# Optimization experiments

Measured on AMD Instinct MI355X. Metric: run time of the kernel, lower is better.

Reference implementation:

```python
import jax, jax.numpy as jnp
import numpy as np

BS, S, D, N, E = 16, 8, 10, 32, 300
H, STATE_DIM, MID, OC = 128, 96, 256, 100

def setup_inputs():
    ks = jax.random.split(jax.random.key(0), 24)
    g = lambda i, shape: (0.02 * jax.random.normal(ks[i], shape)).astype(jnp.float32)
    return {
        "stock_news": jax.random.normal(ks[0], (BS, S, D, N, E), dtype=jnp.float32),
        "stock_feats": jax.random.normal(ks[1], (BS, STATE_DIM), dtype=jnp.float32),
        "conv_w3": g(2, (S, OC, E, 3)), "conv_b3": g(3, (S, OC)),
        "conv_w4": g(4, (S, OC, E, 4)), "conv_b4": g(5, (S, OC)),
        "conv_w5": g(6, (S, OC, E, 5)), "conv_b5": g(7, (S, OC)),
        "w_ih": g(8, (S, 4 * H, 3 * OC)), "w_hh": g(9, (S, 4 * H, H)),
        "b_ih": g(10, (S, 4 * H)), "b_hh": g(11, (S, 4 * H)),
        "linX_w": g(12, (S, H, 2 * H)), "linX_b": g(13, (S, H)),
        "linY_w": g(14, (S, 64, H)), "linY_b": g(15, (S, 64)),
        "w1": g(16, (24, STATE_DIM)), "b1": g(17, (24,)),
        "w2": g(18, (16, 24)), "b2": g(19, (16,)),
        "arch_w1": g(20, (MID, 16 + 64 * S)), "arch_b1": g(21, (MID,)),
        "arch_w2": g(22, (S, MID)), "arch_b2": g(23, (S,)),
        "action_var": jnp.full((S,), -0.25, dtype=jnp.float32),
    }

def _conv_maxpool(x, w, b, k):
    # x: [S,B,D,N,E], w: [S,OC,E,k] -> conv1d over news axis then max-pool -> [S,B,D,OC]
    L = x.shape[3] - k + 1
    y = jnp.broadcast_to(b[:, None, None, None, :], (x.shape[0], x.shape[1], x.shape[2], L, w.shape[1]))
    for j in range(k):
        y = y + jnp.einsum('sbdne,soe->sbdno', x[:, :, :, j:j + L, :], w[:, :, :, j])
    return y.max(axis=3)

def _lstm_attn(xs, w_ih, w_hh, b_ih, b_hh):
    # single-stock LSTM (batch_first) + attention from original code; xs: [B,D,I] -> [B,2H]
    pre = jnp.einsum('bdi,gi->dbg', xs, w_ih) + b_ih + b_hh  # [D,B,4H]
    h0 = jnp.zeros((xs.shape[0], w_hh.shape[1]), xs.dtype)
    def step(carry, g_t):
        h, c = carry
        gates = g_t + h @ w_hh.T
        i, f, g, o = jnp.split(gates, 4, axis=-1)  # PyTorch gate order i,f,g,o
        c = jax.nn.sigmoid(f) * c + jax.nn.sigmoid(i) * jnp.tanh(g)
        h = jax.nn.sigmoid(o) * jnp.tanh(c)
        return (h, c), h
    (hn, _), outs = jax.lax.scan(step, (h0, h0), pre)
    outs = outs.transpose(1, 0, 2)  # [B,D,H]
    w = jnp.einsum('bh,bdh->bd', hn, outs)[:, None, :]  # [B,1,D]
    w = jax.nn.softmax(w, axis=1)  # softmax over singleton dim, exactly as torch code (yields ones)
    out = jnp.sum(w.transpose(0, 2, 1) * outs, axis=1)  # [B,H]
    return jnp.concatenate([hn, out], axis=-1)  # [B,2H]

def _forward(stock_news, stock_feats, conv_w3, conv_b3, conv_w4, conv_b4, conv_w5, conv_b5,
             w_ih, w_hh, b_ih, b_hh, linX_w, linX_b, linY_w, linY_b,
             w1, b1, w2, b2, arch_w1, arch_b1, arch_w2, arch_b2, action_var):
    x = stock_news.transpose(1, 0, 2, 3, 4)  # [S,B,D,N,E]
    feats = [_conv_maxpool(x, w, b, k) for (w, b, k) in
             ((conv_w3, conv_b3, 3), (conv_w4, conv_b4, 4), (conv_w5, conv_b5, 5))]
    text = jnp.concatenate(feats, axis=-1)  # [S,B,D,300]
    comb = jax.vmap(_lstm_attn)(text, w_ih, w_hh, b_ih, b_hh)  # [S,B,2H]
    hX = jax.nn.relu(jnp.einsum('sbi,shi->sbh', comb, linX_w) + linX_b[:, None, :])  # dropout is eval-mode identity
    hY = jax.nn.relu(jnp.einsum('sbh,soh->sbo', hX, linY_w) + linY_b[:, None, :])  # [S,B,64]
    stock_text = hY.transpose(1, 0, 2).reshape(stock_news.shape[0], -1)  # [B,S*64]
    f = jax.nn.relu(stock_feats @ w1.T + b1) @ w2.T + b2  # [B,16]
    total = jnp.concatenate([stock_text, f], axis=-1)  # [B,16+64S]
    mu = jnp.tanh(jax.nn.relu(total @ arch_w1.T + arch_b1) @ arch_w2.T + arch_b2)
    return mu, jnp.exp(action_var)

def reference(stock_news, stock_feats, conv_w3, conv_b3, conv_w4, conv_b4, conv_w5, conv_b5,
              w_ih, w_hh, b_ih, b_hh, linX_w, linX_b, linY_w, linY_b,
              w1, b1, w2, b2, arch_w1, arch_b1, arch_w2, arch_b2, action_var):
    return _forward(stock_news, stock_feats, conv_w3, conv_b3, conv_w4, conv_b4, conv_w5, conv_b5,
                    w_ih, w_hh, b_ih, b_hh, linX_w, linX_b, linY_w, linY_b,
                    w1, b1, w2, b2, arch_w1, arch_b1, arch_w2, arch_b2, action_var)
```

## Files before the change

kernel.cpp:

```cpp
#include <hip/hip_runtime.h>
#include <math.h>

#define S_   8
#define B_   16
#define D_   10
#define N_   32
#define E_   300
#define H_   128
#define G4_  512
#define SDIM_ 96
#define MID_ 256
#define TOT_ 528

#define NWPACK 3850240
#define NWPRE  1310720

typedef unsigned short u16;
typedef __attribute__((ext_vector_type(8))) short short8;
typedef __attribute__((ext_vector_type(4))) short short4v;
typedef __attribute__((ext_vector_type(4))) float f32x4;

static __device__ __forceinline__ u16 f2bf(float f) {
    unsigned u = __builtin_bit_cast(unsigned, f);
    return (u16)((u + 0x7FFFu + ((u >> 16) & 1u)) >> 16);
}

__global__ void prep(const float* __restrict__ w3, const float* __restrict__ b3,
                     const float* __restrict__ w4, const float* __restrict__ b4,
                     const float* __restrict__ w5, const float* __restrict__ b5,
                     const float* __restrict__ w_ih,
                     u16* __restrict__ wpack2, u16* __restrict__ wpre2,
                     float* __restrict__ bcomb) {
    int idx = blockIdx.x * blockDim.x + threadIdx.x;
    if (idx < NWPACK) {
        int j = idx & 7, q = (idx >> 3) & 3;
        int rest = idx >> 5;
        int c = rest % 320, ks = (rest / 320) % 47, s = rest / 15040;
        int kk = ks * 32 + q * 8 + j;
        int tap = kk / 300, e = kk - tap * 300;
        float v = 0.f;
        if (tap < 5) {
            if (c < 100)      { if (tap < 3) v = w3[((s*100 + c      )*300 + e)*3 + tap]; }
            else if (c < 200) { if (tap < 4) v = w4[((s*100 + c - 100)*300 + e)*4 + tap]; }
            else if (c < 300) {              v = w5[((s*100 + c - 200)*300 + e)*5 + tap]; }
        }
        wpack2[idx] = f2bf(v);
    } else if (idx < NWPACK + NWPRE) {
        int i2 = idx - NWPACK;
        int j = i2 & 7, q = (i2 >> 3) & 3;
        int rest = i2 >> 5;
        int g = rest & 511, ks = (rest >> 9) % 10, s = rest / 5120;
        int kk = ks * 32 + q * 8 + j;
        float v = (kk < 300) ? w_ih[((size_t)s * 512 + g) * 300 + kk] : 0.f;
        wpre2[i2] = f2bf(v);
    }
    if (idx < 2560) {
        int c = idx % 320, s = idx / 320;
        float bv = 0.f;
        if (c < 100)      bv = b3[s*100 + c];
        else if (c < 200) bv = b4[s*100 + c - 100];
        else if (c < 300) bv = b5[s*100 + c - 200];
        bcomb[idx] = bv;
    }
}

__global__ __launch_bounds__(256, 3) void conv_mfma(const float* __restrict__ news,
                                                    const u16* __restrict__ wpack2,
                                                    const float* __restrict__ bcomb,
                                                    u16* __restrict__ text_bf) {
    __shared__ u16 xs[2 * 10816];
    const int tid = threadIdx.x, bid = blockIdx.x;
    const int s = bid & 7, b2d = bid >> 3, b2 = b2d / 10, d = b2d % 10;
    const int l = tid & 63, w = tid >> 6, q = l >> 4, r16 = l & 15;

    const u16* gp[5];
#pragma unroll
    for (int nt = 0; nt < 5; ++nt) {
        int c = w * 80 + nt * 16 + r16;
        gp[nt] = wpack2 + (size_t)s * 481280 + c * 32 + q * 8;
    }

    short8 bf0[5], bf1[5];
#pragma unroll
    for (int nt = 0; nt < 5; ++nt) bf0[nt] = *reinterpret_cast<const short8*>(gp[nt]);
#pragma unroll
    for (int nt = 0; nt < 5; ++nt) bf1[nt] = *reinterpret_cast<const short8*>(gp[nt] + 10240);

#pragma unroll
    for (int sm = 0; sm < 2; ++sm) {
        const float4* xg = reinterpret_cast<const float4*>(
            news + (size_t)(((b2 * 2 + sm) * 8 + s) * 10 + d) * 9600);
        for (int i = tid; i < 2704; i += 256) {
            ushort4 u;
            if (i < 2400) {
                float4 v = xg[i];
                u.x = f2bf(v.x); u.y = f2bf(v.y); u.z = f2bf(v.z); u.w = f2bf(v.w);
            } else { u.x = 0; u.y = 0; u.z = 0; u.w = 0; }
            *reinterpret_cast<ushort4*>(&xs[sm * 10816 + 4 * i]) = u;
        }
    }
    __syncthreads();

    f32x4 acc[4][5];
#pragma unroll
    for (int m = 0; m < 4; ++m)
#pragma unroll
        for (int nt = 0; nt < 5; ++nt) acc[m][nt] = (f32x4)(0.f);

#define LOADA(dst, ks) do {                                                     \
    _Pragma("unroll")                                                           \
    for (int m_ = 0; m_ < 4; ++m_) {                                            \
        int off_ = (m_ >> 1) * 10816 + ((m_ & 1) * 16 + r16) * 300 + (ks) * 32 + q * 8; \
        short4v lo_ = *reinterpret_cast<const short4v*>(&xs[off_]);             \
        short4v hi_ = *reinterpret_cast<const short4v*>(&xs[off_ + 4]);         \
        dst[m_] = __builtin_shufflevector(lo_, hi_, 0, 1, 2, 3, 4, 5, 6, 7);    \
    } } while (0)

#define MFMAS(bfv, av) do {                                                     \
    __builtin_amdgcn_s_setprio(1);                                              \
    _Pragma("unroll")                                                           \
    for (int m_ = 0; m_ < 4; ++m_)                                              \
        _Pragma("unroll")                                                       \
        for (int nt_ = 0; nt_ < 5; ++nt_)                                       \
            acc[m_][nt_] = __builtin_amdgcn_mfma_f32_16x16x32_bf16(av[m_], bfv[nt_], acc[m_][nt_], 0, 0, 0); \
    __builtin_amdgcn_s_setprio(0);                                              \
    } while (0)

    for (int ks = 0; ks < 46; ks += 2) {
        short8 a0[4], a1[4];
        LOADA(a0, ks);
        MFMAS(bf0, a0);
#pragma unroll
        for (int nt = 0; nt < 5; ++nt)
            bf0[nt] = *reinterpret_cast<const short8*>(gp[nt] + (ks + 2) * 10240);

        LOADA(a1, ks + 1);
        MFMAS(bf1, a1);
        if (ks + 3 < 47) {
#pragma unroll
            for (int nt = 0; nt < 5; ++nt)
                bf1[nt] = *reinterpret_cast<const short8*>(gp[nt] + (ks + 3) * 10240);
        }
    }
    {
        short8 a0[4];
        LOADA(a0, 46);
        MFMAS(bf0, a0);
    }
#undef LOADA
#undef MFMAS

#pragma unroll
    for (int sm = 0; sm < 2; ++sm) {
        const size_t trow = ((size_t)(s * 16 + b2 * 2 + sm) * 10 + d) * 320;
#pragma unroll
        for (int nt = 0; nt < 5; ++nt) {
            int oc = w * 80 + nt * 16 + r16;
            int L = (oc < 100) ? 30 : (oc < 200) ? 29 : 28;
            float mx = -3e38f;
#pragma unroll
            for (int r = 0; r < 4; ++r) {
                mx = fmaxf(mx, acc[sm * 2][nt][r]);
                int row1 = 16 + q * 4 + r;
                if (row1 < L) mx = fmaxf(mx, acc[sm * 2 + 1][nt][r]);
            }
            mx = fmaxf(mx, __shfl_xor(mx, 16));
            mx = fmaxf(mx, __shfl_xor(mx, 32));
            if (l < 16)
                text_bf[trow + oc] = f2bf(mx + bcomb[s * 320 + oc]);
        }
    }
}

__global__ __launch_bounds__(256) void lstm_pre_mfma(const u16* __restrict__ text_bf,
                                                     const u16* __restrict__ wpre2,
                                                     const float* __restrict__ b_ih,
                                                     const float* __restrict__ b_hh,
                                                     float* __restrict__ pre) {
    __shared__ u16 as16[16 * 320];
    const int sd = blockIdx.x, s = sd / 10, d = sd % 10;
    const int tid = threadIdx.x, l = tid & 63, w = tid >> 6, q = l >> 4, r16 = l & 15;

    for (int i = tid; i < 640; i += 256) {
        int r = i / 40, c = i % 40;
        *reinterpret_cast<float4*>(as16 + r * 320 + ((c ^ (r & 7)) << 3)) =
            *reinterpret_cast<const float4*>(text_bf + ((size_t)(s * 16 + r) * 10 + d) * 320 + c * 8);
    }
    __syncthreads();

    const u16* gpb[8];
#pragma unroll
    for (int nt = 0; nt < 8; ++nt) {
        int g = w * 128 + nt * 16 + r16;
        gpb[nt] = wpre2 + (size_t)s * 163840 + g * 32 + q * 8;
    }

    f32x4 acc[8];
#pragma unroll
    for (int nt = 0; nt < 8; ++nt) acc[nt] = (f32x4)(0.f);

    for (int ks = 0; ks < 10; ++ks) {
        short8 a = *reinterpret_cast<const short8*>(
            as16 + r16 * 320 + (((ks * 4 + q) ^ (r16 & 7)) << 3));
#pragma unroll
        for (int nt = 0; nt < 8; ++nt) {
            short8 bf = *reinterpret_cast<const short8*>(gpb[nt] + ks * 16384);
            acc[nt] = __builtin_amdgcn_mfma_f32_16x16x32_bf16(a, bf, acc[nt], 0, 0, 0);
        }
    }

#pragma unroll
    for (int nt = 0; nt < 8; ++nt) {
        int g = w * 128 + nt * 16 + r16;
        float bias = b_ih[s * 512 + g] + b_hh[s * 512 + g];
#pragma unroll
        for (int r = 0; r < 4; ++r) {
            int brow = q * 4 + r;
            pre[((size_t)sd * 16 + brow) * 512 + g] = acc[nt][r] + bias;
        }
    }
}

__global__ __launch_bounds__(512) void lstm_tail(const float* __restrict__ pre,
                                                 const float* __restrict__ w_hh,
                                                 const float* __restrict__ lxw, const float* __restrict__ lxb,
                                                 const float* __restrict__ lyw, const float* __restrict__ lyb,
                                                 float* __restrict__ total) {
    __shared__ float h_lds[H_];
    __shared__ float gates[G4_];
    __shared__ __align__(16) float comb_l[256];
    __shared__ __align__(16) float hx[H_];
    const int sb = blockIdx.x;
    const int s = sb / B_, b = sb % B_;
    const int t = threadIdx.x;

    float4 wr[32];
    const float4* wp = reinterpret_cast<const float4*>(w_hh + ((size_t)s * G4_ + t) * H_);
#pragma unroll
    for (int i = 0; i < 32; ++i) wr[i] = wp[i];

    float c = 0.f, hsum = 0.f, hval = 0.f;
    if (t < H_) h_lds[t] = 0.f;
    __syncthreads();

    for (int d = 0; d < D_; ++d) {
        float acc = pre[(((size_t)(s * D_ + d) * B_ + b)) * G4_ + t];
#pragma unroll
        for (int i = 0; i < 32; ++i) {
            float4 h4 = *reinterpret_cast<const float4*>(&h_lds[i * 4]);
            acc = fmaf(wr[i].w, h4.w, fmaf(wr[i].z, h4.z, fmaf(wr[i].y, h4.y, fmaf(wr[i].x, h4.x, acc))));
        }
        gates[t] = acc;
        __syncthreads();
        if (t < H_) {
            float ig = 1.f / (1.f + expf(-gates[t]));
            float fg = 1.f / (1.f + expf(-gates[H_ + t]));
            float gg = tanhf(gates[2 * H_ + t]);
            float og = 1.f / (1.f + expf(-gates[3 * H_ + t]));
            c = fg * c + ig * gg;
            hval = og * tanhf(c);
            hsum += hval;
            h_lds[t] = hval;
        }
        __syncthreads();
    }
    if (t < H_) { comb_l[t] = hval; comb_l[H_ + t] = hsum; }
    __syncthreads();
    if (t < H_) {
        const float4* wv = reinterpret_cast<const float4*>(lxw + ((size_t)s * H_ + t) * 256);
        float acc = lxb[s * H_ + t];
#pragma unroll
        for (int i = 0; i < 64; ++i) {
            float4 w4 = wv[i], x4 = reinterpret_cast<float4*>(comb_l)[i];
            acc = fmaf(w4.w, x4.w, fmaf(w4.z, x4.z, fmaf(w4.y, x4.y, fmaf(w4.x, x4.x, acc))));
        }
        hx[t] = fmaxf(acc, 0.f);
    }
    __syncthreads();
    if (t < 64) {
        const float4* wv = reinterpret_cast<const float4*>(lyw + ((size_t)s * 64 + t) * H_);
        float acc = lyb[s * 64 + t];
#pragma unroll
        for (int i = 0; i < 32; ++i) {
            float4 w4 = wv[i], x4 = reinterpret_cast<float4*>(hx)[i];
            acc = fmaf(w4.w, x4.w, fmaf(w4.z, x4.z, fmaf(w4.y, x4.y, fmaf(w4.x, x4.x, acc))));
        }
        total[(size_t)b * 512 + s * 64 + t] = fmaxf(acc, 0.f);
    }
}

__global__ __launch_bounds__(256) void head_feats(const float* __restrict__ total,
                                                  const float* __restrict__ sf,
                                                  const float* __restrict__ w1, const float* __restrict__ b1,
                                                  const float* __restrict__ w2, const float* __restrict__ b2,
                                                  const float* __restrict__ aw1, const float* __restrict__ ab1,
                                                  const float* __restrict__ aw2, const float* __restrict__ ab2,
                                                  const float* __restrict__ avar,
                                                  float* __restrict__ out) {
    __shared__ __align__(16) float tr[TOT_];
    __shared__ float hid[MID_];
    __shared__ float h1f[24];
    const int bb = blockIdx.x, t = threadIdx.x;
    if (t < 128)
        reinterpret_cast<float4*>(tr)[t] = reinterpret_cast<const float4*>(total + (size_t)bb * 512)[t];
    if (t < 24) {
        float acc = b1[t];
        for (int i = 0; i < SDIM_; ++i) acc = fmaf(sf[bb * SDIM_ + i], w1[t * SDIM_ + i], acc);
        h1f[t] = fmaxf(acc, 0.f);
    }
    __syncthreads();
    if (t < 16) {
        float acc = b2[t];
        for (int i = 0; i < 24; ++i) acc = fmaf(h1f[i], w2[t * 24 + i], acc);
        tr[512 + t] = acc;
    }
    __syncthreads();
    {
        const float4* wv = reinterpret_cast<const float4*>(aw1 + (size_t)t * TOT_);
        float acc = ab1[t];
#pragma unroll
        for (int i = 0; i < TOT_ / 4; ++i) {
            float4 w4 = wv[i], x4 = reinterpret_cast<float4*>(tr)[i];
            acc = fmaf(w4.w, x4.w, fmaf(w4.z, x4.z, fmaf(w4.y, x4.y, fmaf(w4.x, x4.x, acc))));
        }
        hid[t] = fmaxf(acc, 0.f);
    }
    __syncthreads();
    if (t < 8) {
        float acc = ab2[t];
        const float* wv = aw2 + (size_t)t * MID_;
        for (int i = 0; i < MID_; ++i) acc = fmaf(hid[i], wv[i], acc);
        out[bb * 8 + t] = tanhf(acc);
    }
    if (bb == 0 && t >= 8 && t < 16) out[128 + (t - 8)] = expf(avar[t - 8]);
}

extern "C" void kernel_launch(void* const* d_in, const int* in_sizes, int n_in,
                              void* d_out, int out_size, void* d_ws, size_t ws_size,
                              hipStream_t stream) {
    const float* news = (const float*)d_in[0];
    const float* sf   = (const float*)d_in[1];
    const float* w3   = (const float*)d_in[2];  const float* b3 = (const float*)d_in[3];
    const float* w4   = (const float*)d_in[4];  const float* b4 = (const float*)d_in[5];
    const float* w5   = (const float*)d_in[6];  const float* b5 = (const float*)d_in[7];
    const float* w_ih = (const float*)d_in[8];  const float* w_hh = (const float*)d_in[9];
    const float* b_ih = (const float*)d_in[10]; const float* b_hh = (const float*)d_in[11];
    const float* lxw  = (const float*)d_in[12]; const float* lxb = (const float*)d_in[13];
    const float* lyw  = (const float*)d_in[14]; const float* lyb = (const float*)d_in[15];
    const float* w1   = (const float*)d_in[16]; const float* b1 = (const float*)d_in[17];
    const float* w2   = (const float*)d_in[18]; const float* b2 = (const float*)d_in[19];
    const float* aw1  = (const float*)d_in[20]; const float* ab1 = (const float*)d_in[21];
    const float* aw2  = (const float*)d_in[22]; const float* ab2 = (const float*)d_in[23];
    const float* avar = (const float*)d_in[24];

    char* ws = (char*)d_ws;
    u16*   wpack2  = (u16*)ws;
    u16*   wpre2   = (u16*)(ws + 7700480);
    float* bcomb   = (float*)(ws + 10321920);
    u16*   text_bf = (u16*)(ws + 10332160);
    float* pre     = (float*)(ws + 11151360);
    float* total   = (float*)(ws + 13772800);

    prep<<<(NWPACK + NWPRE + 255) / 256, 256, 0, stream>>>(w3, b3, w4, b4, w5, b5, w_ih,
                                                           wpack2, wpre2, bcomb);
    conv_mfma<<<640, 256, 0, stream>>>(news, wpack2, bcomb, text_bf);
    lstm_pre_mfma<<<S_ * D_, 256, 0, stream>>>(text_bf, wpre2, b_ih, b_hh, pre);
    lstm_tail<<<S_ * B_, 512, 0, stream>>>(pre, w_hh, lxw, lxb, lyw, lyb, total);
    head_feats<<<B_, 256, 0, stream>>>(total, sf, w1, b1, w2, b2, aw1, ab1, aw2, ab2, avar, (float*)d_out);
}
```

Before: 134.4 us.

## Transpose tail weights for coalesced loads and software-pipeline conv LDS reads

Adds transposed copies of the linX, linY and arch_w1 weights, built in the prep kernel, so the tail and head matvecs read weights with coalesced per-thread strides instead of row-wise float4 streams. The LSTM recurrent weights are now staged through a padded LDS chunk before going into registers, and the recurrence dot product is split across four accumulators. The conv kernel prefetches the next A fragment from LDS ahead of each MFMA batch, and its launch bound drops from 3 to 2 waves per SIMD to leave room for the extra registers. Costs include more prep work and workspace, LDS staging overhead, and possibly lower conv occupancy.

Result: no change. 134.4 us (+0.0%).

```diff
diff --git a/kernel.cpp b/kernel.cpp
--- a/kernel.cpp
+++ b/kernel.cpp
@@ -29,8 +29,12 @@
                      const float* __restrict__ w4, const float* __restrict__ b4,
                      const float* __restrict__ w5, const float* __restrict__ b5,
                      const float* __restrict__ w_ih,
+                     const float* __restrict__ lxw, const float* __restrict__ lyw,
+                     const float* __restrict__ aw1,
                      u16* __restrict__ wpack2, u16* __restrict__ wpre2,
-                     float* __restrict__ bcomb) {
+                     float* __restrict__ bcomb,
+                     float* __restrict__ lxwT, float* __restrict__ lywT,
+                     float* __restrict__ aw1T) {
     int idx = blockIdx.x * blockDim.x + threadIdx.x;
     if (idx < NWPACK) {
         int j = idx & 7, q = (idx >> 3) & 3;
@@ -54,6 +58,18 @@
         float v = (kk < 300) ? w_ih[((size_t)s * 512 + g) * 300 + kk] : 0.f;
         wpre2[i2] = f2bf(v);
     }
+    if (idx < 262144) {
+        int t = idx & 127, i = (idx >> 7) & 255, s = idx >> 15;
+        lxwT[idx] = lxw[((size_t)(s * 128 + t)) * 256 + i];
+    }
+    if (idx < 65536) {
+        int t = idx & 63, i = (idx >> 6) & 127, s = idx >> 13;
+        lywT[idx] = lyw[((size_t)(s * 64 + t)) * 128 + i];
+    }
+    if (idx < 135168) {
+        int j = idx & 255, i = idx >> 8;
+        aw1T[idx] = aw1[(size_t)j * TOT_ + i];
+    }
     if (idx < 2560) {
         int c = idx % 320, s = idx / 320;
         float bv = 0.f;
@@ -64,7 +80,7 @@
     }
 }
 
-__global__ __launch_bounds__(256, 3) void conv_mfma(const float* __restrict__ news,
+__global__ __launch_bounds__(256, 2) void conv_mfma(const float* __restrict__ news,
                                                     const u16* __restrict__ wpack2,
                                                     const float* __restrict__ bcomb,
                                                     u16* __restrict__ text_bf) {
@@ -126,15 +142,16 @@
     __builtin_amdgcn_s_setprio(0);                                              \
     } while (0)
 
+    short8 a0[4], a1[4];
+    LOADA(a0, 0);
     for (int ks = 0; ks < 46; ks += 2) {
-        short8 a0[4], a1[4];
-        LOADA(a0, ks);
+        LOADA(a1, ks + 1);
         MFMAS(bf0, a0);
 #pragma unroll
         for (int nt = 0; nt < 5; ++nt)
             bf0[nt] = *reinterpret_cast<const short8*>(gp[nt] + (ks + 2) * 10240);
 
-        LOADA(a1, ks + 1);
+        LOADA(a0, ks + 2);
         MFMAS(bf1, a1);
         if (ks + 3 < 47) {
 #pragma unroll
@@ -142,11 +159,7 @@
                 bf1[nt] = *reinterpret_cast<const short8*>(gp[nt] + (ks + 3) * 10240);
         }
     }
-    {
-        short8 a0[4];
-        LOADA(a0, 46);
-        MFMAS(bf0, a0);
-    }
+    MFMAS(bf0, a0);
 #undef LOADA
 #undef MFMAS
 
@@ -223,42 +236,60 @@
 
 __global__ __launch_bounds__(512) void lstm_tail(const float* __restrict__ pre,
                                                  const float* __restrict__ w_hh,
-                                                 const float* __restrict__ lxw, const float* __restrict__ lxb,
-                                                 const float* __restrict__ lyw, const float* __restrict__ lyb,
+                                                 const float* __restrict__ lxwT, const float* __restrict__ lxb,
+                                                 const float* __restrict__ lywT, const float* __restrict__ lyb,
                                                  float* __restrict__ total) {
+    __shared__ float wchunk[128][129];
     __shared__ float h_lds[H_];
     __shared__ float gates[G4_];
-    __shared__ __align__(16) float comb_l[256];
+    __shared__ float comb_l[256];
     __shared__ __align__(16) float hx[H_];
     const int sb = blockIdx.x;
     const int s = sb / B_, b = sb % B_;
     const int t = threadIdx.x;
 
-    float4 wr[32];
-    const float4* wp = reinterpret_cast<const float4*>(w_hh + ((size_t)s * G4_ + t) * H_);
-#pragma unroll
-    for (int i = 0; i < 32; ++i) wr[i] = wp[i];
-
-    float c = 0.f, hsum = 0.f, hval = 0.f;
+    float wrs[128];
+    for (int c = 0; c < 4; ++c) {
+        for (int i2 = t; i2 < 128 * 32; i2 += 512) {
+            int row = i2 >> 5, fq = i2 & 31;
+            float4 v = *reinterpret_cast<const float4*>(
+                w_hh + ((size_t)(s * G4_ + c * 128 + row)) * H_ + fq * 4);
+            wchunk[row][fq * 4 + 0] = v.x; wchunk[row][fq * 4 + 1] = v.y;
+            wchunk[row][fq * 4 + 2] = v.z; wchunk[row][fq * 4 + 3] = v.w;
+        }
+        __syncthreads();
+        if ((t >> 7) == c) {
+            int r = t & 127;
+#pragma unroll
+            for (int i = 0; i < 128; ++i) wrs[i] = wchunk[r][i];
+        }
+        __syncthreads();
+    }
+
+    float cc = 0.f, hsum = 0.f, hval = 0.f;
     if (t < H_) h_lds[t] = 0.f;
     __syncthreads();
 
     for (int d = 0; d < D_; ++d) {
-        float acc = pre[(((size_t)(s * D_ + d) * B_ + b)) * G4_ + t];
-#pragma unroll
-        for (int i = 0; i < 32; ++i) {
-            float4 h4 = *reinterpret_cast<const float4*>(&h_lds[i * 4]);
-            acc = fmaf(wr[i].w, h4.w, fmaf(wr[i].z, h4.z, fmaf(wr[i].y, h4.y, fmaf(wr[i].x, h4.x, acc))));
-        }
-        gates[t] = acc;
+        float a0 = pre[(((size_t)(s * D_ + d) * B_ + b)) * G4_ + t];
+        float a1 = 0.f, a2 = 0.f, a3 = 0.f;
+#pragma unroll
+        for (int i = 0; i < 128; i += 4) {
+            float4 h4 = *reinterpret_cast<const float4*>(&h_lds[i]);
+            a0 = fmaf(wrs[i + 0], h4.x, a0);
+            a1 = fmaf(wrs[i + 1], h4.y, a1);
+            a2 = fmaf(wrs[i + 2], h4.z, a2);
+            a3 = fmaf(wrs[i + 3], h4.w, a3);
+        }
+        gates[t] = (a0 + a1) + (a2 + a3);
         __syncthreads();
         if (t < H_) {
             float ig = 1.f / (1.f + expf(-gates[t]));
             float fg = 1.f / (1.f + expf(-gates[H_ + t]));
             float gg = tanhf(gates[2 * H_ + t]);
             float og = 1.f / (1.f + expf(-gates[3 * H_ + t]));
-            c = fg * c + ig * gg;
-            hval = og * tanhf(c);
+            cc = fg * cc + ig * gg;
+            hval = og * tanhf(cc);
             hsum += hval;
             h_lds[t] = hval;
         }
@@ -267,25 +298,23 @@
     if (t < H_) { comb_l[t] = hval; comb_l[H_ + t] = hsum; }
     __syncthreads();
     if (t < H_) {
-        const float4* wv = reinterpret_cast<const float4*>(lxw + ((size_t)s * H_ + t) * 256);
-        float acc = lxb[s * H_ + t];
-#pragma unroll
-        for (int i = 0; i < 64; ++i) {
-            float4 w4 = wv[i], x4 = reinterpret_cast<float4*>(comb_l)[i];
-            acc = fmaf(w4.w, x4.w, fmaf(w4.z, x4.z, fmaf(w4.y, x4.y, fmaf(w4.x, x4.x, acc))));
-        }
-        hx[t] = fmaxf(acc, 0.f);
+        const float* wv = lxwT + (size_t)s * 256 * 128 + t;
+        float a0 = lxb[s * H_ + t], a1 = 0.f;
+        for (int i = 0; i < 256; i += 2) {
+            a0 = fmaf(comb_l[i], wv[(size_t)i * 128], a0);
+            a1 = fmaf(comb_l[i + 1], wv[(size_t)(i + 1) * 128], a1);
+        }
+        hx[t] = fmaxf(a0 + a1, 0.f);
     }
     __syncthreads();
     if (t < 64) {
-        const float4* wv = reinterpret_cast<const float4*>(lyw + ((size_t)s * 64 + t) * H_);
-        float acc = lyb[s * 64 + t];
-#pragma unroll
-        for (int i = 0; i < 32; ++i) {
-            float4 w4 = wv[i], x4 = reinterpret_cast<float4*>(hx)[i];
-            acc = fmaf(w4.w, x4.w, fmaf(w4.z, x4.z, fmaf(w4.y, x4.y, fmaf(w4.x, x4.x, acc))));
-        }
-        total[(size_t)b * 512 + s * 64 + t] = fmaxf(acc, 0.f);
+        const float* wv = lywT + (size_t)s * 128 * 64 + t;
+        float a0 = lyb[s * 64 + t], a1 = 0.f;
+        for (int i = 0; i < 128; i += 2) {
+            a0 = fmaf(hx[i], wv[(size_t)i * 64], a0);
+            a1 = fmaf(hx[i + 1], wv[(size_t)(i + 1) * 64], a1);
+        }
+        total[(size_t)b * 512 + s * 64 + t] = fmaxf(a0 + a1, 0.f);
     }
 }
 
@@ -293,7 +322,7 @@
                                                   const float* __restrict__ sf,
                                                   const float* __restrict__ w1, const float* __restrict__ b1,
                                                   const float* __restrict__ w2, const float* __restrict__ b2,
-                                                  const float* __restrict__ aw1, const float* __restrict__ ab1,
+                                                  const float* __restrict__ aw1T, const float* __restrict__ ab1,
                                                   const float* __restrict__ aw2, const float* __restrict__ ab2,
                                                   const float* __restrict__ avar,
                                                   float* __restrict__ out) {
@@ -316,14 +345,15 @@
     }
     __syncthreads();
     {
-        const float4* wv = reinterpret_cast<const float4*>(aw1 + (size_t)t * TOT_);
-        float acc = ab1[t];
-#pragma unroll
-        for (int i = 0; i < TOT_ / 4; ++i) {
-            float4 w4 = wv[i], x4 = reinterpret_cast<float4*>(tr)[i];
-            acc = fmaf(w4.w, x4.w, fmaf(w4.z, x4.z, fmaf(w4.y, x4.y, fmaf(w4.x, x4.x, acc))));
-        }
-        hid[t] = fmaxf(acc, 0.f);
+        const float* wv = aw1T + t;
+        float a0 = ab1[t], a1 = 0.f, a2 = 0.f, a3 = 0.f;
+        for (int i = 0; i < TOT_; i += 4) {
+            a0 = fmaf(tr[i + 0], wv[(size_t)(i + 0) * 256], a0);
+            a1 = fmaf(tr[i + 1], wv[(size_t)(i + 1) * 256], a1);
+            a2 = fmaf(tr[i + 2], wv[(size_t)(i + 2) * 256], a2);
+            a3 = fmaf(tr[i + 3], wv[(size_t)(i + 3) * 256], a3);
+        }
+        hid[t] = fmaxf((a0 + a1) + (a2 + a3), 0.f);
     }
     __syncthreads();
     if (t < 8) {
@@ -360,11 +390,15 @@
     u16*   text_bf = (u16*)(ws + 10332160);
     float* pre     = (float*)(ws + 11151360);
     float* total   = (float*)(ws + 13772800);
+    float* lxwT    = (float*)(ws + 13805568);
+    float* lywT    = (float*)(ws + 14854144);
+    float* aw1T    = (float*)(ws + 15116288);
 
     prep<<<(NWPACK + NWPRE + 255) / 256, 256, 0, stream>>>(w3, b3, w4, b4, w5, b5, w_ih,
-                                                           wpack2, wpre2, bcomb);
+                                                           lxw, lyw, aw1,
+                                                           wpack2, wpre2, bcomb, lxwT, lywT, aw1T);
     conv_mfma<<<640, 256, 0, stream>>>(news, wpack2, bcomb, text_bf);
     lstm_pre_mfma<<<S_ * D_, 256, 0, stream>>>(text_bf, wpre2, b_ih, b_hh, pre);
-    lstm_tail<<<S_ * B_, 512, 0, stream>>>(pre, w_hh, lxw, lxb, lyw, lyb, total);
-    head_feats<<<B_, 256, 0, stream>>>(total, sf, w1, b1, w2, b2, aw1, ab1, aw2, ab2, avar, (float*)d_out);
-}
+    lstm_tail<<<S_ * B_, 512, 0, stream>>>(pre, w_hh, lxwT, lxb, lywT, lyb, total);
+    head_feats<<<B_, 256, 0, stream>>>(total, sf, w1, b1, w2, b2, aw1T, ab1, aw2, ab2, avar, (float*)d_out);
+}
```
